# Optimization experiments

Hardware: AMD Instinct MI355X
Metric: run time of the kernel (lower is better)

The kernel has to match this reference:

```python
import jax, jax.numpy as jnp
import numpy as np
from jax import lax

B, N, HC = 16, 4096, 64
EPS = 1e-5


def _fps(xyz, npoint):
    # xyz: [B,N,3] -> indices [B,npoint]; deterministic start at index 0
    b, n, _ = xyz.shape
    def step(carry, _):
        dist, far = carry
        centroid = jnp.take_along_axis(xyz, far[:, None, None], axis=1)  # [B,1,3]
        d = jnp.sum((xyz - centroid) ** 2, -1)                           # [B,N]
        dist = jnp.minimum(dist, d)
        nxt = jnp.argmax(dist, -1).astype(jnp.int32)
        return (dist, nxt), far
    init = (jnp.full((b, n), 1e10, xyz.dtype), jnp.zeros((b,), jnp.int32))
    _, idx = lax.scan(step, init, None, length=npoint)
    return idx.T


def _index_points(pts, idx):
    # pts [B,N,C], idx [B,...] int -> [B,...,C]
    b = idx.shape[0]
    flat = jnp.take_along_axis(pts, idx.reshape(b, -1)[..., None], axis=1)
    return flat.reshape(idx.shape + (pts.shape[-1],))


def _ball_query(radius, nsample, xyz, new_xyz):
    # torch square_distance: ||a||^2 + ||b||^2 - 2 a.b
    n = xyz.shape[1]
    sqr = (jnp.sum(new_xyz ** 2, -1)[:, :, None] + jnp.sum(xyz ** 2, -1)[:, None, :]
           - 2.0 * jnp.einsum('bsd,bnd->bsn', new_xyz, xyz))          # [B,S,N]
    gi = jnp.where(sqr > radius ** 2, n, jnp.arange(n, dtype=jnp.int32))
    gi = jnp.sort(gi, axis=-1)[:, :, :nsample]
    first = gi[:, :, :1]
    return jnp.where(gi == n, first, gi)


def _mlp_maxpool(x, params):
    # x: [B,S,K,C]; 1x1 conv == per-point matmul; BN in training mode (batch stats)
    for (w, bb, g, be) in params:
        x = jnp.einsum('bskc,cd->bskd', x, w) + bb
        m = jnp.mean(x, axis=(0, 1, 2))
        v = jnp.var(x, axis=(0, 1, 2))
        x = g * (x - m) * lax.rsqrt(v + EPS) + be
        x = jax.nn.relu(x)
    return jnp.max(x, axis=2)  # [B,S,Cout]


def _sa(xyz, points, npoint, radius, nsample, params, group_all):
    # xyz [B,3,N], points [B,D,N] (channel-first, like torch)
    xyzt = jnp.transpose(xyz, (0, 2, 1))
    ptst = jnp.transpose(points, (0, 2, 1))
    if group_all:
        new_xyz = jnp.zeros((xyzt.shape[0], 1, 3), xyzt.dtype)
        new_pts = jnp.concatenate([xyzt[:, None], ptst[:, None]], -1)  # [B,1,N,3+D]
    else:
        fidx = _fps(xyzt, npoint)
        new_xyz = _index_points(xyzt, fidx)                            # [B,S,3]
        gi = _ball_query(radius, nsample, xyzt, new_xyz)               # [B,S,K]
        gxyz = _index_points(xyzt, gi) - new_xyz[:, :, None]           # [B,S,K,3]
        new_pts = jnp.concatenate([gxyz, _index_points(ptst, gi)], -1)
    feat = _mlp_maxpool(new_pts, params)                               # [B,S,Cout]
    return jnp.transpose(new_xyz, (0, 2, 1)), jnp.transpose(feat, (0, 2, 1))


def setup_inputs() -> dict:
    key = jax.random.key(0)
    ks = jax.random.split(key, 8)
    inp = {
        'l0_xyz': jax.random.normal(ks[0], (B, 3, N), jnp.float32),
        'l0_points': jax.random.normal(ks[1], (B, 3, N), jnp.float32),
    }
    dims = {'sa1': [(6, HC), (HC, HC * 2)],
            'sa2': [(HC * 2 + 3, HC * 2), (HC * 2, HC * 4)],
            'sa3': [(HC * 4 + 3, HC * 4), (HC * 4, HC * 8)]}
    i = 2
    for name, layers in dims.items():
        for j, (cin, cout) in enumerate(layers, 1):
            inp[f'{name}_w{j}'] = jax.random.normal(ks[i], (cin, cout), jnp.float32) * (1.0 / np.sqrt(cin))
            inp[f'{name}_b{j}'] = jnp.zeros((cout,), jnp.float32)
            inp[f'{name}_g{j}'] = jnp.ones((cout,), jnp.float32)
            inp[f'{name}_be{j}'] = jnp.zeros((cout,), jnp.float32)
            i += 1
    return inp


def reference(l0_xyz, l0_points,
              sa1_w1, sa1_b1, sa1_g1, sa1_be1, sa1_w2, sa1_b2, sa1_g2, sa1_be2,
              sa2_w1, sa2_b1, sa2_g1, sa2_be1, sa2_w2, sa2_b2, sa2_g2, sa2_be2,
              sa3_w1, sa3_b1, sa3_g1, sa3_be1, sa3_w2, sa3_b2, sa3_g2, sa3_be2):
    p1 = [(sa1_w1, sa1_b1, sa1_g1, sa1_be1), (sa1_w2, sa1_b2, sa1_g2, sa1_be2)]
    p2 = [(sa2_w1, sa2_b1, sa2_g1, sa2_be1), (sa2_w2, sa2_b2, sa2_g2, sa2_be2)]
    p3 = [(sa3_w1, sa3_b1, sa3_g1, sa3_be1), (sa3_w2, sa3_b2, sa3_g2, sa3_be2)]
    l1_xyz, l1_points = _sa(l0_xyz, l0_points, 256, 0.2, 32, p1, False)
    l2_xyz, l2_points = _sa(l1_xyz, l1_points, 128, 0.25, 64, p2, False)
    l3_xyz, l3_points = _sa(l2_xyz, l2_points, None, None, None, p3, True)
    x = l3_points.reshape(-1, HC * 8)
    return (l1_xyz, l1_points, l2_xyz, l2_points, l3_xyz, x)
```

## Files before the change

kernel.cpp:

```cpp
#include <hip/hip_runtime.h>
#include <cstddef>


#define EPSB 1e-5f
constexpr int SLOTS1 = 16;
constexpr int SLOTS2 = 64;
constexpr int BATCH = 16;

static __device__ __forceinline__ unsigned long long umax64(unsigned long long a,
                                                            unsigned long long b)
{
    return a > b ? a : b;
}

static __device__ __forceinline__ unsigned pack_bf16x2(float a, float b)
{
    unsigned ua = __float_as_uint(a), ub = __float_as_uint(b);
    ua += 0x7fffu + ((ua >> 16) & 1u);
    ub += 0x7fffu + ((ub >> 16) & 1u);
    return (ua >> 16) | (ub & 0xffff0000u);
}

static __device__ __forceinline__ unsigned short bf16_of(float a)
{
    unsigned u = __float_as_uint(a);
    u += 0x7fffu + ((u >> 16) & 1u);
    return (unsigned short)(u >> 16);
}

static __device__ __forceinline__ unsigned long long wave_umax64_dpp(unsigned long long x)
{
#define DPP_STEP(ctrl, rmask)                                                        \
    {                                                                                \
        int lo_ = __builtin_amdgcn_update_dpp(0, (int)(unsigned)x, ctrl, rmask, 0xf, false); \
        int hi_ = __builtin_amdgcn_update_dpp(0, (int)(unsigned)(x >> 32), ctrl, rmask, 0xf, false); \
        unsigned long long c_ = ((unsigned long long)(unsigned)hi_ << 32) | (unsigned)lo_; \
        x = umax64(x, c_);                                                           \
    }
    DPP_STEP(0x111, 0xf)
    DPP_STEP(0x112, 0xf)
    DPP_STEP(0x114, 0xf)
    DPP_STEP(0x118, 0xf)
    DPP_STEP(0x142, 0xa)
    DPP_STEP(0x143, 0xc)
#undef DPP_STEP
    unsigned lo = (unsigned)__builtin_amdgcn_readlane((int)(unsigned)x, 63);
    unsigned hi = (unsigned)__builtin_amdgcn_readlane((int)(unsigned)(x >> 32), 63);
    return ((unsigned long long)hi << 32) | lo;
}

template<int N, int NPOINT, int THREADS>
__device__ __forceinline__ void fps_body(char* smraw,
        const float* __restrict__ xyz, int bStride, int cStride, int nStride,
        int b, float* __restrict__ nxyz, float* __restrict__ lxyz)
{
    constexpr int PT = N / THREADS;
    constexpr int NW = THREADS / 64;
    const int t = threadIdx.x;
    float* sx = (float*)smraw;
    float* sy = sx + N;
    float* sz = sy + N;
    int* sel = (int*)(sz + N);
    unsigned long long* red = (unsigned long long*)(sel + NPOINT);
    const float* xb = xyz + (size_t)b * bStride;

    float px[PT], py[PT], pz[PT], dist[PT];
#pragma unroll
    for (int i = 0; i < PT; ++i) {
        int p = t + i * THREADS;
        px[i] = xb[(size_t)0 * cStride + (size_t)p * nStride];
        py[i] = xb[(size_t)1 * cStride + (size_t)p * nStride];
        pz[i] = xb[(size_t)2 * cStride + (size_t)p * nStride];
        sx[p] = px[i]; sy[p] = py[i]; sz[p] = pz[i];
        dist[i] = 1e10f;
    }
    if (t == 0) sel[0] = 0;
    if constexpr (NW > 1) __syncthreads();

    float cx = sx[0], cy = sy[0], cz = sz[0];
    for (int it = 1; it < NPOINT; ++it) {
        unsigned long long best = 0ull;
#pragma unroll
        for (int i = 0; i < PT; ++i) {
            float dx = px[i] - cx, dy = py[i] - cy, dz = pz[i] - cz;
            float d = __builtin_fmaf(dx, dx, __builtin_fmaf(dy, dy, dz * dz));
            float nd = fminf(dist[i], d);
            dist[i] = nd;
            unsigned long long k =
                ((unsigned long long)__float_as_uint(nd) << 32) |
                (unsigned int)(~(t + i * THREADS));
            best = umax64(best, k);
        }
        best = wave_umax64_dpp(best);
        int widx;
        if constexpr (NW > 1) {
            const int pb = it & 1;
            if ((t & 63) == 0) red[pb * NW + (t >> 6)] = best;
            __syncthreads();
            unsigned long long m = red[pb * NW + 0];
#pragma unroll
            for (int w = 1; w < NW; ++w) m = umax64(m, red[pb * NW + w]);
            widx = (int)(~(unsigned int)m);
        } else {
            widx = (int)(~(unsigned int)best);
        }
        if (t == 0) sel[it] = widx;
        cx = sx[widx]; cy = sy[widx]; cz = sz[widx];
    }
    if constexpr (NW > 1) __syncthreads();
    for (int s = t; s < NPOINT; s += THREADS) {
        int id = sel[s];
        float X = sx[id], Y = sy[id], Z = sz[id];
        nxyz[(size_t)(b * NPOINT + s) * 3 + 0] = X;
        nxyz[(size_t)(b * NPOINT + s) * 3 + 1] = Y;
        nxyz[(size_t)(b * NPOINT + s) * 3 + 2] = Z;
        lxyz[(size_t)b * 3 * NPOINT + 0 * NPOINT + s] = X;
        lxyz[(size_t)b * 3 * NPOINT + 1 * NPOINT + s] = Y;
        lxyz[(size_t)b * 3 * NPOINT + 2 * NPOINT + s] = Z;
    }
}

template<int COUTB>
__device__ __forceinline__ void proj_gemm_body(char* smraw, int blk,
        const float* __restrict__ xyzsrc, const float* __restrict__ featsrc,
        int N, int CF, const float* __restrict__ W, int coutFull,
        const float* __restrict__ bias, float* __restrict__ outp)
{
    constexpr int BK = 32, BKP = 36, TK = 4, TC = 4, THREADS = 512, ROWS = 64;
    constexpr int C2G = COUTB / TC;
    static_assert(C2G * (ROWS / TK) == THREADS, "thread shape");
    float (*al)[BKP] = (float (*)[BKP])smraw;
    float (*wl)[BKP] = (float (*)[BKP])(smraw + ROWS * BKP * 4);
    const int NCH = coutFull / COUTB;
    const int chunk = blk % NCH;
    const int rb = blk / NCH;
    const int m0 = rb * ROWS;
    const int c2_0 = chunk * COUTB;
    const int K = CF + 3;
    const int tid = threadIdx.x;
    const int c2g = tid % C2G, kt = tid / C2G;
    float acc[TK][TC];
#pragma unroll
    for (int i = 0; i < TK; ++i)
#pragma unroll
        for (int j = 0; j < TC; ++j) acc[i][j] = 0.f;
    const int npan = (K + BK - 1) / BK;
    for (int pan = 0; pan < npan; ++pan) {
        __syncthreads();
        const int cbase = pan * BK;
        for (int e = tid; e < ROWS * BK; e += THREADS) {
            int rl = e / BK, cl = e % BK;
            int c = cbase + cl;
            int m = m0 + rl;
            int bb = m / N, n = m % N;
            float v = 0.f;
            if (c < 3) v = xyzsrc[(size_t)(bb * N + n) * 3 + c];
            else if (c < K) v = featsrc[(size_t)(bb * N + n) * CF + (c - 3)];
            al[rl][cl] = v;
        }
        for (int e = tid; e < COUTB * BK; e += THREADS) {
            int c2 = e % COUTB, cl = e / COUTB;
            int c = cbase + cl;
            wl[c2][cl] = (c < K) ? W[(size_t)c * coutFull + c2_0 + c2] : 0.f;
        }
        __syncthreads();
#pragma unroll
        for (int cl = 0; cl < BK; cl += 4) {
            float4 av[TK], wv[TC];
#pragma unroll
            for (int i = 0; i < TK; ++i) av[i] = *(const float4*)&al[kt * TK + i][cl];
#pragma unroll
            for (int j = 0; j < TC; ++j) wv[j] = *(const float4*)&wl[c2g + j * C2G][cl];
#pragma unroll
            for (int i = 0; i < TK; ++i)
#pragma unroll
                for (int j = 0; j < TC; ++j)
                    acc[i][j] += av[i].x * wv[j].x + av[i].y * wv[j].y
                               + av[i].z * wv[j].z + av[i].w * wv[j].w;
        }
    }
#pragma unroll
    for (int j = 0; j < TC; ++j) {
        float bb_ = bias[c2_0 + c2g + j * C2G];
#pragma unroll
        for (int i = 0; i < TK; ++i) {
            int m = m0 + kt * TK + i;
            outp[(size_t)m * coutFull + c2_0 + c2g + j * C2G] = acc[i][j] + bb_;
        }
    }
}

__global__ __launch_bounds__(512)
void mega1_kernel(const float* __restrict__ l0_xyz, const float* __restrict__ l0_pts,
                  const float* __restrict__ w11, const float* __restrict__ b11,
                  float* __restrict__ p1,
                  float* __restrict__ nxyz1, float* __restrict__ o_l1xyz,
                  const float* __restrict__ w12, unsigned short* __restrict__ w12t,
                  const float* __restrict__ w22, unsigned short* __restrict__ w22t,
                  const float* __restrict__ w32, unsigned short* __restrict__ w32t,
                  float* __restrict__ stats)
{
    __shared__ __attribute__((aligned(16))) char arena[50304];
    int blk = blockIdx.x;
    const int tid = threadIdx.x;
    if (blk < 16) {
        fps_body<4096, 256, 512>(arena, l0_xyz, 3 * 4096, 4096, 1, blk, nxyz1, o_l1xyz);
        return;
    }
    blk -= 16;
    if (blk < 8192) {
        int idx = blk * 512 + tid;
        int d = idx & 63;
        int n = (idx >> 6) & 4095;
        int b = idx >> 18;
        const float* xb = l0_xyz + (size_t)b * 3 * 4096 + n;
        const float* pb = l0_pts + (size_t)b * 3 * 4096 + n;
        float a0 = xb[0], a1 = xb[4096], a2 = xb[2 * 4096];
        float a3 = pb[0], a4 = pb[4096], a5 = pb[2 * 4096];
        float acc = b11[d];
        acc += a0 * w11[d] + a1 * w11[64 + d] + a2 * w11[128 + d];
        acc += a3 * w11[192 + d] + a4 * w11[256 + d] + a5 * w11[320 + d];
        p1[idx] = acc;
        return;
    }
    blk -= 8192;
    if (blk < 16) {
        int i = blk * 512 + tid;
        if (i < 64 * 128) { int k = i / 128, n = i % 128; w12t[(size_t)n * 64 + k] = bf16_of(w12[i]); }
        return;
    }
    blk -= 16;
    if (blk < 64) {
        int i = blk * 512 + tid;
        if (i < 128 * 256) { int k = i / 256, n = i % 256; w22t[(size_t)n * 128 + k] = bf16_of(w22[i]); }
        return;
    }
    blk -= 64;
    if (blk < 256) {
        int i = blk * 512 + tid;
        if (i < 256 * 512) { int k = i / 512, n = i % 512; w32t[(size_t)n * 256 + k] = bf16_of(w32[i]); }
        return;
    }
    blk -= 256;
    {
        int i = blk * 512 + tid;
        if (i < 129024) stats[i] = 0.f;
    }
}

__global__ __launch_bounds__(512)
void mega2_kernel(const float* __restrict__ nxyz1, float* __restrict__ nxyz2,
                  float* __restrict__ o_l2xyz,
                  const float* __restrict__ feat1, const float* __restrict__ w21,
                  const float* __restrict__ b21, float* __restrict__ p2)
{
    __shared__ __attribute__((aligned(16))) char arena[27648];
    if (blockIdx.x < 16) {
        if (threadIdx.x < 64)
            fps_body<256, 128, 64>(arena, nxyz1, 768, 1, 3, blockIdx.x, nxyz2, o_l2xyz);
        return;
    }
    proj_gemm_body<128>(arena, blockIdx.x - 16, nxyz1, feat1, 256, 128, w21, 128, b21, p2);
}

__global__ __launch_bounds__(512)
void proj_gemm3_kernel(const float* __restrict__ xyzsrc, const float* __restrict__ featsrc,
                       int N, int CF, const float* __restrict__ W, int coutFull,
                       const float* __restrict__ bias, float* __restrict__ outp)
{
    __shared__ __attribute__((aligned(16))) char arena[27648];
    proj_gemm_body<128>(arena, blockIdx.x, xyzsrc, featsrc, N, CF, W, coutFull, bias, outp);
}

template<int NS, int D>
__global__ __launch_bounds__(64)
void ballstat_kernel(const float* __restrict__ xyz, int bStride, int cStride, int nStride, int N,
                     const float* __restrict__ nxyz, int S, float r2,
                     int* __restrict__ gi,
                     const float* __restrict__ W, float* __restrict__ q,
                     const float* __restrict__ p, float* __restrict__ slots)
{
    constexpr int DL = D / 64;
    __shared__ int sgo[NS];
    int bs = blockIdx.x;
    int b = bs / S;
    int l = threadIdx.x;
    float cx = nxyz[(size_t)bs * 3 + 0], cy = nxyz[(size_t)bs * 3 + 1], cz = nxyz[(size_t)bs * 3 + 2];
    float s2 = cx * cx + cy * cy + cz * cz;
    const float* xb = xyz + (size_t)b * bStride;
    int cnt = 0;
    int first = N - 1;
    int* go = gi + (size_t)bs * NS;
    for (int base = 0; base < N; base += 64) {
        int n = base + l;
        float x = xb[(size_t)0 * cStride + (size_t)n * nStride];
        float y = xb[(size_t)1 * cStride + (size_t)n * nStride];
        float z = xb[(size_t)2 * cStride + (size_t)n * nStride];
        float x2 = x * x + y * y + z * z;
        float dot = cx * x + cy * y + cz * z;
        float sqr = (s2 + x2) - 2.0f * dot;
        bool pass = (sqr <= r2);
        unsigned long long m = __ballot(pass);
        if (cnt == 0 && m) first = base + (__ffsll((unsigned long long)m) - 1);
        int pos = cnt + __popcll(m & ((1ull << l) - 1ull));
        if (pass && pos < NS) { go[pos] = n; sgo[pos] = n; }
        cnt += __popcll(m);
        if (cnt >= NS) break;
    }
    if (cnt < NS && l >= cnt && l < NS) { go[l] = first; sgo[l] = first; }

    float qv[DL];
#pragma unroll
    for (int j = 0; j < DL; ++j) {
        int d = j * 64 + l;
        qv[j] = cx * W[d] + cy * W[D + d] + cz * W[2 * D + d];
        q[(size_t)bs * D + d] = qv[j];
    }

    float s[DL], ss[DL];
#pragma unroll
    for (int j = 0; j < DL; ++j) { s[j] = 0.f; ss[j] = 0.f; }
    for (int k = 0; k < NS; ++k) {
        int idx = sgo[k];
        const float* pr = p + (size_t)(b * N + idx) * D;
#pragma unroll
        for (int j = 0; j < DL; ++j) {
            float v = pr[j * 64 + l] - qv[j];
            s[j] += v; ss[j] += v * v;
        }
    }
    int slot = bs & (SLOTS1 - 1);
#pragma unroll
    for (int j = 0; j < DL; ++j) {
        int d = j * 64 + l;
        atomicAdd(&slots[(size_t)(slot * 2 + 0) * D + d], s[j]);
        atomicAdd(&slots[(size_t)(slot * 2 + 1) * D + d], ss[j]);
    }
}

__global__ __launch_bounds__(256)
void stats_raw_kernel(const float* __restrict__ h, int M, int C, float* __restrict__ slots)
{
    int c = threadIdx.x;
    float sum = 0.f, sq = 0.f;
    for (int m = blockIdx.x; m < M; m += gridDim.x) {
        float v = h[(size_t)m * C + c];
        sum += v; sq += v * v;
    }
    int slot = blockIdx.x & (SLOTS1 - 1);
    atomicAdd(&slots[(size_t)(slot * 2 + 0) * C + c], sum);
    atomicAdd(&slots[(size_t)(slot * 2 + 1) * C + c], sq);
}

__global__ __launch_bounds__(256)
void bnfin_kernel(const float* __restrict__ st, int C, float cnt,
                  const float* __restrict__ g, const float* __restrict__ be,
                  float* __restrict__ sc, float* __restrict__ sh)
{
    int c = blockIdx.x * 256 + threadIdx.x;
    if (c >= C) return;
    float s0 = 0.f, s1 = 0.f;
    for (int sl = 0; sl < SLOTS1; ++sl) {
        s0 += st[(size_t)(sl * 2 + 0) * C + c];
        s1 += st[(size_t)(sl * 2 + 1) * C + c];
    }
    float mean = s0 / cnt;
    float var = s1 / cnt - mean * mean;
    float inv = 1.0f / sqrtf(var + EPSB);
    float s = g[c] * inv;
    sc[c] = s;
    sh[c] = be[c] - s * mean;
}

template<int KS, int CIN, int COUTB>
__global__ __launch_bounds__(512)
void mfma_gemm_kernel(const float* __restrict__ p, const float* __restrict__ q,
                      const int* __restrict__ gi, int S, int NCH, int N,
                      const float* __restrict__ bnsc, const float* __restrict__ bnsh,
                      const unsigned short* __restrict__ w2t, int coutFull,
                      const float* __restrict__ b2,
                      float* __restrict__ st2,
                      float* __restrict__ mx, float* __restrict__ mn)
{
    constexpr int MT = KS / 16;
    constexpr int NSL = 8 / MT;
    constexpr int SLW = COUTB / NSL;
    constexpr int TPW = SLW / 16;
    constexpr int KST = CIN / 32;
    constexpr int LDA = CIN + 8;
    typedef __attribute__((ext_vector_type(8))) short bf16x8;
    typedef __attribute__((ext_vector_type(4))) float f32x4;

    __shared__ __attribute__((aligned(16))) unsigned short hl[KS][LDA];
    __shared__ float red[4][8][SLW];

    const int chunk = blockIdx.x % NCH;
    const int bs = blockIdx.x / NCH;
    const int b = bs / S;
    const int tid = threadIdx.x;
    const int c2_0 = chunk * COUTB;
    const int w = tid >> 6, lane = tid & 63;
    const int mt = w % MT, ns = w / MT;
    const int lrow = lane & 15, quad = lane >> 4;

    constexpr int ITER = KS * CIN / (512 * 4);
    const int gbase = bs * KS;
#pragma unroll
    for (int it = 0; it < ITER; ++it) {
        int e = (it * 512 + tid) * 4;
        int k = e / CIN, c = e % CIN;
        int row = gi ? (b * N + gi[gbase + k]) : (b * KS + k);
        float4 v = *(const float4*)&p[(size_t)row * CIN + c];
        if (q) {
            float4 qq = *(const float4*)&q[(size_t)bs * CIN + c];
            v.x -= qq.x; v.y -= qq.y; v.z -= qq.z; v.w -= qq.w;
        }
        float4 sc = *(const float4*)&bnsc[c];
        float4 sh = *(const float4*)&bnsh[c];
        v.x = fmaxf(__builtin_fmaf(sc.x, v.x, sh.x), 0.f);
        v.y = fmaxf(__builtin_fmaf(sc.y, v.y, sh.y), 0.f);
        v.z = fmaxf(__builtin_fmaf(sc.z, v.z, sh.z), 0.f);
        v.w = fmaxf(__builtin_fmaf(sc.w, v.w, sh.w), 0.f);
        uint2 pk;
        pk.x = pack_bf16x2(v.x, v.y);
        pk.y = pack_bf16x2(v.z, v.w);
        *(uint2*)&hl[k][c] = pk;
    }
    __syncthreads();

    f32x4 acc[TPW];
#pragma unroll
    for (int t = 0; t < TPW; ++t) acc[t] = (f32x4){0.f, 0.f, 0.f, 0.f};

    const int nbase = c2_0 + ns * SLW + lrow;
#pragma unroll
    for (int ks = 0; ks < KST; ++ks) {
        bf16x8 a = *(const bf16x8*)&hl[mt * 16 + lrow][ks * 32 + quad * 8];
#pragma unroll
        for (int t = 0; t < TPW; ++t) {
            bf16x8 bfr = *(const bf16x8*)&w2t[(size_t)(nbase + t * 16) * CIN + ks * 32 + quad * 8];
            acc[t] = __builtin_amdgcn_mfma_f32_16x16x32_bf16(a, bfr, acc[t], 0, 0, 0);
        }
    }

#pragma unroll
    for (int t = 0; t < TPW; ++t) {
        float bias = b2[nbase + t * 16];
        float s = 0.f, sq = 0.f, amx = -3.4e38f, amn = 3.4e38f;
#pragma unroll
        for (int r = 0; r < 4; ++r) {
            float v = acc[t][r] + bias;
            s += v; sq += v * v;
            amx = fmaxf(amx, v); amn = fminf(amn, v);
        }
#pragma unroll
        for (int off = 16; off < 64; off <<= 1) {
            s += __shfl_xor(s, off);
            sq += __shfl_xor(sq, off);
            amx = fmaxf(amx, __shfl_xor(amx, off));
            amn = fminf(amn, __shfl_xor(amn, off));
        }
        if (quad == 0) {
            int lc = t * 16 + lrow;
            red[0][w][lc] = s; red[1][w][lc] = sq;
            red[2][w][lc] = amx; red[3][w][lc] = amn;
        }
    }
    __syncthreads();
    for (int c = tid; c < COUTB; c += 512) {
        int ns2 = c / SLW, lc = c % SLW;
        float s = 0.f, sq = 0.f, amx = -3.4e38f, amn = 3.4e38f;
#pragma unroll
        for (int m2 = 0; m2 < MT; ++m2) {
            int w2 = ns2 * MT + m2;
            s += red[0][w2][lc]; sq += red[1][w2][lc];
            amx = fmaxf(amx, red[2][w2][lc]);
            amn = fminf(amn, red[3][w2][lc]);
        }
        int slot = blockIdx.x & (SLOTS2 - 1);
        atomicAdd(&st2[(size_t)(slot * 2 + 0) * coutFull + c2_0 + c], s);
        atomicAdd(&st2[(size_t)(slot * 2 + 1) * coutFull + c2_0 + c], sq);
        mx[(size_t)bs * coutFull + c2_0 + c] = amx;
        mn[(size_t)bs * coutFull + c2_0 + c] = amn;
    }
}

__global__ __launch_bounds__(256)
void apply_kernel(const float* __restrict__ st2, int C, float m2count,
                  const float* __restrict__ g2, const float* __restrict__ be2,
                  const float* __restrict__ mx, const float* __restrict__ mn,
                  int S, float* __restrict__ feat, float* __restrict__ outT,
                  int total, float* __restrict__ zero48)
{
    __shared__ float sc[512], sh[512];
    for (int c = threadIdx.x; c < C; c += 256) {
        float s0 = 0.f, s1 = 0.f;
        for (int sl = 0; sl < SLOTS2; ++sl) {
            s0 += st2[(size_t)(sl * 2 + 0) * C + c];
            s1 += st2[(size_t)(sl * 2 + 1) * C + c];
        }
        float mean = s0 / m2count;
        float var = s1 / m2count - mean * mean;
        float inv = 1.0f / sqrtf(var + EPSB);
        float scl = g2[c] * inv;
        sc[c] = scl; sh[c] = be2[c] - scl * mean;
    }
    __syncthreads();
    if (zero48 && blockIdx.x == 0 && threadIdx.x < 48) zero48[threadIdx.x] = 0.f;
    for (int e = blockIdx.x * 256 + threadIdx.x; e < total; e += gridDim.x * 256) {
        int c = e % C;
        int s = (e / C) % S;
        int b = e / (C * S);
        float scl = sc[c];
        float v = (scl >= 0.f) ? mx[e] : mn[e];
        float y = fmaxf(scl * v + sh[c], 0.f);
        if (feat) feat[e] = y;
        outT[((size_t)b * C + c) * S + s] = y;
    }
}

extern "C" void kernel_launch(void* const* d_in, const int* in_sizes, int n_in,
                              void* d_out, int out_size, void* d_ws, size_t ws_size,
                              hipStream_t stream)
{
    (void)in_sizes; (void)n_in; (void)out_size; (void)ws_size;
    const float* l0_xyz = (const float*)d_in[0];
    const float* l0_pts = (const float*)d_in[1];
    const float* w11 = (const float*)d_in[2];  const float* b11 = (const float*)d_in[3];
    const float* g11 = (const float*)d_in[4];  const float* be11 = (const float*)d_in[5];
    const float* w12 = (const float*)d_in[6];  const float* b12 = (const float*)d_in[7];
    const float* g12 = (const float*)d_in[8];  const float* be12 = (const float*)d_in[9];
    const float* w21 = (const float*)d_in[10]; const float* b21 = (const float*)d_in[11];
    const float* g21 = (const float*)d_in[12]; const float* be21 = (const float*)d_in[13];
    const float* w22 = (const float*)d_in[14]; const float* b22 = (const float*)d_in[15];
    const float* g22 = (const float*)d_in[16]; const float* be22 = (const float*)d_in[17];
    const float* w31 = (const float*)d_in[18]; const float* b31 = (const float*)d_in[19];
    const float* g31 = (const float*)d_in[20]; const float* be31 = (const float*)d_in[21];
    const float* w32 = (const float*)d_in[22]; const float* b32 = (const float*)d_in[23];
    const float* g32 = (const float*)d_in[24]; const float* be32 = (const float*)d_in[25];

    float* out = (float*)d_out;
    float* o_l1xyz = out;
    float* o_l1pts = out + 12288;
    float* o_l2xyz = out + 536576;
    float* o_l2pts = out + 542720;
    float* o_l3xyz = out + 1067008;
    float* o_x     = out + 1067056;

    char* ws = (char*)d_ws;
    size_t off = 0;
    auto alloc = [&](size_t bytes) {
        void* r = ws + off;
        off += ((bytes + 255) & ~(size_t)255);
        return r;
    };
    float* nxyz1 = (float*)alloc(12288 * 4);
    float* nxyz2 = (float*)alloc(6144 * 4);
    int*   gi1   = (int*)alloc(131072 * 4);
    int*   gi2   = (int*)alloc(131072 * 4);
    float* p1    = (float*)alloc(4194304 * 4);
    float* q1    = (float*)alloc(262144 * 4);
    float* feat1 = (float*)alloc(524288 * 4);
    float* mx1   = (float*)alloc(524288 * 4);
    float* mn1   = (float*)alloc(524288 * 4);
    float* p2    = (float*)alloc(524288 * 4);
    float* q2    = (float*)alloc(262144 * 4);
    float* feat2 = (float*)alloc(524288 * 4);
    float* mx2   = (float*)alloc(524288 * 4);
    float* mn2   = (float*)alloc(524288 * 4);
    float* h31   = (float*)alloc(524288 * 4);
    float* mx3   = (float*)alloc(8192 * 4);
    float* mn3   = (float*)alloc(8192 * 4);
    float* stats = (float*)alloc(129024 * 4);
    float* st1a = stats;
    float* st2a = st1a + 2048;
    float* st1b = st2a + 16384;
    float* st2b = st1b + 4096;
    float* st3a = st2b + 32768;
    float* st3b = st3a + 8192;
    unsigned short* w12t = (unsigned short*)alloc(128 * 64 * 2);
    unsigned short* w22t = (unsigned short*)alloc(256 * 128 * 2);
    unsigned short* w32t = (unsigned short*)alloc(512 * 256 * 2);
    float* sc1 = (float*)alloc(64 * 4);   float* sh1 = (float*)alloc(64 * 4);
    float* sc2 = (float*)alloc(128 * 4);  float* sh2 = (float*)alloc(128 * 4);
    float* sc3 = (float*)alloc(256 * 4);  float* sh3 = (float*)alloc(256 * 4);

    mega1_kernel<<<8796, 512, 0, stream>>>(l0_xyz, l0_pts, w11, b11, p1,
                                           nxyz1, o_l1xyz,
                                           w12, w12t, w22, w22t, w32, w32t, stats);
    ballstat_kernel<32, 64><<<4096, 64, 0, stream>>>(l0_xyz, 3 * 4096, 4096, 1, 4096,
                                                     nxyz1, 256, 0.04f, gi1, w11, q1, p1, st1a);
    bnfin_kernel<<<1, 256, 0, stream>>>(st1a, 64, 131072.0f, g11, be11, sc1, sh1);
    mfma_gemm_kernel<32, 64, 128><<<4096, 512, 0, stream>>>(
        p1, q1, gi1, 256, 1, 4096, sc1, sh1, w12t, 128, b12, st2a, mx1, mn1);
    apply_kernel<<<128, 256, 0, stream>>>(st2a, 128, 131072.0f, g12, be12, mx1, mn1,
                                          256, feat1, o_l1pts, 524288, nullptr);

    mega2_kernel<<<80, 512, 0, stream>>>(nxyz1, nxyz2, o_l2xyz, feat1, w21, b21, p2);
    ballstat_kernel<64, 128><<<2048, 64, 0, stream>>>(nxyz1, 768, 1, 3, 256,
                                                      nxyz2, 128, 0.0625f, gi2, w21, q2, p2, st1b);
    bnfin_kernel<<<1, 256, 0, stream>>>(st1b, 128, 131072.0f, g21, be21, sc2, sh2);
    mfma_gemm_kernel<64, 128, 256><<<2048, 512, 0, stream>>>(
        p2, q2, gi2, 128, 1, 256, sc2, sh2, w22t, 256, b22, st2b, mx2, mn2);
    apply_kernel<<<128, 256, 0, stream>>>(st2b, 256, 131072.0f, g22, be22, mx2, mn2,
                                          128, feat2, o_l2pts, 524288, nullptr);

    proj_gemm3_kernel<<<64, 512, 0, stream>>>(nxyz2, feat2, 128, 256, w31, 256, b31, h31);
    stats_raw_kernel<<<128, 256, 0, stream>>>(h31, 2048, 256, st3a);
    bnfin_kernel<<<1, 256, 0, stream>>>(st3a, 256, 2048.0f, g31, be31, sc3, sh3);
    mfma_gemm_kernel<128, 256, 128><<<64, 512, 0, stream>>>(
        h31, nullptr, nullptr, 1, 4, 0, sc3, sh3, w32t, 512, b32, st3b, mx3, mn3);
    apply_kernel<<<32, 256, 0, stream>>>(st3b, 512, 2048.0f, g32, be32, mx3, mn3,
                                         1, nullptr, o_x, 8192, o_l3xyz);
}
```

Measured before the change: 567.2 us.

## Fuse BN finalize, apply and projection kernels; register-resident FPS with coordinate broadcast

FPS now tracks each candidate's coordinates in registers and passes the winning point's xyz through a small shared slot or readlane. This removes the shared-memory point arrays and the index-then-lookup step. The second-level FPS moves into the first ball-query launch, and BN finalization is folded into the GEMM and apply kernels, which removes the bnfin launches. The BN apply for each level is fused into the next level's projection GEMM together with its stats accumulation, dropping the feat buffers and the stats_raw kernel, which cuts launch count and intermediate traffic. In exchange, several blocks each recompute the BN scale/shift from the slot sums, and launch_bounds occupancy hints are added.

```diff
diff --git a/kernel.cpp b/kernel.cpp
--- a/kernel.cpp
+++ b/kernel.cpp
@@ -5,7 +5,6 @@
 #define EPSB 1e-5f
 constexpr int SLOTS1 = 16;
 constexpr int SLOTS2 = 64;
-constexpr int BATCH = 16;
 
 static __device__ __forceinline__ unsigned long long umax64(unsigned long long a,
                                                             unsigned long long b)
@@ -50,18 +49,15 @@
 }
 
 template<int N, int NPOINT, int THREADS>
-__device__ __forceinline__ void fps_body(char* smraw,
+__device__ __forceinline__ void fps_body(
+        unsigned long long* kslots, float4* cslots,
         const float* __restrict__ xyz, int bStride, int cStride, int nStride,
         int b, float* __restrict__ nxyz, float* __restrict__ lxyz)
 {
     constexpr int PT = N / THREADS;
     constexpr int NW = THREADS / 64;
+    constexpr int NSTASH = (NPOINT + THREADS - 1) / THREADS;
     const int t = threadIdx.x;
-    float* sx = (float*)smraw;
-    float* sy = sx + N;
-    float* sz = sy + N;
-    int* sel = (int*)(sz + N);
-    unsigned long long* red = (unsigned long long*)(sel + NPOINT);
     const float* xb = xyz + (size_t)b * bStride;
 
     float px[PT], py[PT], pz[PT], dist[PT];
@@ -71,126 +67,80 @@
         px[i] = xb[(size_t)0 * cStride + (size_t)p * nStride];
         py[i] = xb[(size_t)1 * cStride + (size_t)p * nStride];
         pz[i] = xb[(size_t)2 * cStride + (size_t)p * nStride];
-        sx[p] = px[i]; sy[p] = py[i]; sz[p] = pz[i];
         dist[i] = 1e10f;
     }
-    if (t == 0) sel[0] = 0;
-    if constexpr (NW > 1) __syncthreads();
-
-    float cx = sx[0], cy = sy[0], cz = sz[0];
+    float stx[NSTASH], sty[NSTASH], stz[NSTASH];
+#pragma unroll
+    for (int i = 0; i < NSTASH; ++i) { stx[i] = 0.f; sty[i] = 0.f; stz[i] = 0.f; }
+
+    float cx = xb[0], cy = xb[(size_t)cStride], cz = xb[(size_t)2 * cStride];
+    if (t == 0) { stx[0] = cx; sty[0] = cy; stz[0] = cz; }
+
     for (int it = 1; it < NPOINT; ++it) {
-        unsigned long long best = 0ull;
+        float bv = -1.0f; int bidx = 0; float bx = 0.f, by = 0.f, bz = 0.f;
 #pragma unroll
         for (int i = 0; i < PT; ++i) {
             float dx = px[i] - cx, dy = py[i] - cy, dz = pz[i] - cz;
             float d = __builtin_fmaf(dx, dx, __builtin_fmaf(dy, dy, dz * dz));
             float nd = fminf(dist[i], d);
             dist[i] = nd;
-            unsigned long long k =
-                ((unsigned long long)__float_as_uint(nd) << 32) |
-                (unsigned int)(~(t + i * THREADS));
-            best = umax64(best, k);
-        }
-        best = wave_umax64_dpp(best);
-        int widx;
+            bool g = nd > bv;
+            bv = g ? nd : bv;
+            bidx = g ? (t + i * THREADS) : bidx;
+            bx = g ? px[i] : bx; by = g ? py[i] : by; bz = g ? pz[i] : bz;
+        }
+        unsigned long long mykey =
+            ((unsigned long long)__float_as_uint(bv) << 32) | (unsigned)(~bidx);
+        unsigned long long wkey = wave_umax64_dpp(mykey);
+        float wx, wy, wz;
         if constexpr (NW > 1) {
             const int pb = it & 1;
-            if ((t & 63) == 0) red[pb * NW + (t >> 6)] = best;
+            if (mykey == wkey) {
+                kslots[pb * NW + (t >> 6)] = wkey;
+                cslots[pb * NW + (t >> 6)] = make_float4(bx, by, bz, 0.f);
+            }
             __syncthreads();
-            unsigned long long m = red[pb * NW + 0];
-#pragma unroll
-            for (int w = 1; w < NW; ++w) m = umax64(m, red[pb * NW + w]);
-            widx = (int)(~(unsigned int)m);
+            unsigned long long k[NW]; float4 cc[NW];
+#pragma unroll
+            for (int w = 0; w < NW; ++w) { k[w] = kslots[pb * NW + w]; cc[w] = cslots[pb * NW + w]; }
+#pragma unroll
+            for (int stp = 1; stp < NW; stp <<= 1)
+#pragma unroll
+                for (int w = 0; w < NW; w += 2 * stp)
+                    if (k[w + stp] > k[w]) { k[w] = k[w + stp]; cc[w] = cc[w + stp]; }
+            wkey = k[0]; wx = cc[0].x; wy = cc[0].y; wz = cc[0].z;
         } else {
-            widx = (int)(~(unsigned int)best);
-        }
-        if (t == 0) sel[it] = widx;
-        cx = sx[widx]; cy = sy[widx]; cz = sz[widx];
-    }
-    if constexpr (NW > 1) __syncthreads();
-    for (int s = t; s < NPOINT; s += THREADS) {
-        int id = sel[s];
-        float X = sx[id], Y = sy[id], Z = sz[id];
-        nxyz[(size_t)(b * NPOINT + s) * 3 + 0] = X;
-        nxyz[(size_t)(b * NPOINT + s) * 3 + 1] = Y;
-        nxyz[(size_t)(b * NPOINT + s) * 3 + 2] = Z;
-        lxyz[(size_t)b * 3 * NPOINT + 0 * NPOINT + s] = X;
-        lxyz[(size_t)b * 3 * NPOINT + 1 * NPOINT + s] = Y;
-        lxyz[(size_t)b * 3 * NPOINT + 2 * NPOINT + s] = Z;
-    }
-}
-
-template<int COUTB>
-__device__ __forceinline__ void proj_gemm_body(char* smraw, int blk,
-        const float* __restrict__ xyzsrc, const float* __restrict__ featsrc,
-        int N, int CF, const float* __restrict__ W, int coutFull,
-        const float* __restrict__ bias, float* __restrict__ outp)
-{
-    constexpr int BK = 32, BKP = 36, TK = 4, TC = 4, THREADS = 512, ROWS = 64;
-    constexpr int C2G = COUTB / TC;
-    static_assert(C2G * (ROWS / TK) == THREADS, "thread shape");
-    float (*al)[BKP] = (float (*)[BKP])smraw;
-    float (*wl)[BKP] = (float (*)[BKP])(smraw + ROWS * BKP * 4);
-    const int NCH = coutFull / COUTB;
-    const int chunk = blk % NCH;
-    const int rb = blk / NCH;
-    const int m0 = rb * ROWS;
-    const int c2_0 = chunk * COUTB;
-    const int K = CF + 3;
-    const int tid = threadIdx.x;
-    const int c2g = tid % C2G, kt = tid / C2G;
-    float acc[TK][TC];
-#pragma unroll
-    for (int i = 0; i < TK; ++i)
-#pragma unroll
-        for (int j = 0; j < TC; ++j) acc[i][j] = 0.f;
-    const int npan = (K + BK - 1) / BK;
-    for (int pan = 0; pan < npan; ++pan) {
-        __syncthreads();
-        const int cbase = pan * BK;
-        for (int e = tid; e < ROWS * BK; e += THREADS) {
-            int rl = e / BK, cl = e % BK;
-            int c = cbase + cl;
-            int m = m0 + rl;
-            int bb = m / N, n = m % N;
-            float v = 0.f;
-            if (c < 3) v = xyzsrc[(size_t)(bb * N + n) * 3 + c];
-            else if (c < K) v = featsrc[(size_t)(bb * N + n) * CF + (c - 3)];
-            al[rl][cl] = v;
-        }
-        for (int e = tid; e < COUTB * BK; e += THREADS) {
-            int c2 = e % COUTB, cl = e / COUTB;
-            int c = cbase + cl;
-            wl[c2][cl] = (c < K) ? W[(size_t)c * coutFull + c2_0 + c2] : 0.f;
-        }
-        __syncthreads();
-#pragma unroll
-        for (int cl = 0; cl < BK; cl += 4) {
-            float4 av[TK], wv[TC];
-#pragma unroll
-            for (int i = 0; i < TK; ++i) av[i] = *(const float4*)&al[kt * TK + i][cl];
-#pragma unroll
-            for (int j = 0; j < TC; ++j) wv[j] = *(const float4*)&wl[c2g + j * C2G][cl];
-#pragma unroll
-            for (int i = 0; i < TK; ++i)
-#pragma unroll
-                for (int j = 0; j < TC; ++j)
-                    acc[i][j] += av[i].x * wv[j].x + av[i].y * wv[j].y
-                               + av[i].z * wv[j].z + av[i].w * wv[j].w;
-        }
-    }
-#pragma unroll
-    for (int j = 0; j < TC; ++j) {
-        float bb_ = bias[c2_0 + c2g + j * C2G];
-#pragma unroll
-        for (int i = 0; i < TK; ++i) {
-            int m = m0 + kt * TK + i;
-            outp[(size_t)m * coutFull + c2_0 + c2g + j * C2G] = acc[i][j] + bb_;
-        }
-    }
-}
-
-__global__ __launch_bounds__(512)
+            unsigned long long ball = __ballot(mykey == wkey);
+            int wl = __ffsll(ball) - 1;
+            wx = __int_as_float(__builtin_amdgcn_readlane(__float_as_int(bx), wl));
+            wy = __int_as_float(__builtin_amdgcn_readlane(__float_as_int(by), wl));
+            wz = __int_as_float(__builtin_amdgcn_readlane(__float_as_int(bz), wl));
+        }
+        if constexpr (NSTASH == 1) {
+            if (t == it) { stx[0] = wx; sty[0] = wy; stz[0] = wz; }
+        } else {
+            if ((it & (THREADS - 1)) == t) {
+                if (it >= THREADS) { stx[1] = wx; sty[1] = wy; stz[1] = wz; }
+                else               { stx[0] = wx; sty[0] = wy; stz[0] = wz; }
+            }
+        }
+        cx = wx; cy = wy; cz = wz;
+    }
+#pragma unroll
+    for (int s2 = 0; s2 < NSTASH; ++s2) {
+        int s = t + s2 * THREADS;
+        if (s < NPOINT) {
+            nxyz[(size_t)(b * NPOINT + s) * 3 + 0] = stx[s2];
+            nxyz[(size_t)(b * NPOINT + s) * 3 + 1] = sty[s2];
+            nxyz[(size_t)(b * NPOINT + s) * 3 + 2] = stz[s2];
+            lxyz[(size_t)b * 3 * NPOINT + 0 * NPOINT + s] = stx[s2];
+            lxyz[(size_t)b * 3 * NPOINT + 1 * NPOINT + s] = sty[s2];
+            lxyz[(size_t)b * 3 * NPOINT + 2 * NPOINT + s] = stz[s2];
+        }
+    }
+}
+
+__global__ __launch_bounds__(512, 2)
 void mega1_kernel(const float* __restrict__ l0_xyz, const float* __restrict__ l0_pts,
                   const float* __restrict__ w11, const float* __restrict__ b11,
                   float* __restrict__ p1,
@@ -200,11 +150,12 @@
                   const float* __restrict__ w32, unsigned short* __restrict__ w32t,
                   float* __restrict__ stats)
 {
-    __shared__ __attribute__((aligned(16))) char arena[50304];
+    __shared__ unsigned long long kxs[16];
+    __shared__ float4 cxs[16];
     int blk = blockIdx.x;
     const int tid = threadIdx.x;
     if (blk < 16) {
-        fps_body<4096, 256, 512>(arena, l0_xyz, 3 * 4096, 4096, 1, blk, nxyz1, o_l1xyz);
+        fps_body<4096, 256, 512>(kxs, cxs, l0_xyz, 3 * 4096, 4096, 1, blk, nxyz1, o_l1xyz);
         return;
     }
     blk -= 16;
@@ -248,41 +199,25 @@
     }
 }
 
-__global__ __launch_bounds__(512)
-void mega2_kernel(const float* __restrict__ nxyz1, float* __restrict__ nxyz2,
-                  float* __restrict__ o_l2xyz,
-                  const float* __restrict__ feat1, const float* __restrict__ w21,
-                  const float* __restrict__ b21, float* __restrict__ p2)
-{
-    __shared__ __attribute__((aligned(16))) char arena[27648];
-    if (blockIdx.x < 16) {
-        if (threadIdx.x < 64)
-            fps_body<256, 128, 64>(arena, nxyz1, 768, 1, 3, blockIdx.x, nxyz2, o_l2xyz);
-        return;
-    }
-    proj_gemm_body<128>(arena, blockIdx.x - 16, nxyz1, feat1, 256, 128, w21, 128, b21, p2);
-}
-
-__global__ __launch_bounds__(512)
-void proj_gemm3_kernel(const float* __restrict__ xyzsrc, const float* __restrict__ featsrc,
-                       int N, int CF, const float* __restrict__ W, int coutFull,
-                       const float* __restrict__ bias, float* __restrict__ outp)
-{
-    __shared__ __attribute__((aligned(16))) char arena[27648];
-    proj_gemm_body<128>(arena, blockIdx.x, xyzsrc, featsrc, N, CF, W, coutFull, bias, outp);
-}
-
-template<int NS, int D>
-__global__ __launch_bounds__(64)
+template<int NS, int D, bool WITHFPS>
+__global__ __launch_bounds__(64, 4)
 void ballstat_kernel(const float* __restrict__ xyz, int bStride, int cStride, int nStride, int N,
                      const float* __restrict__ nxyz, int S, float r2,
                      int* __restrict__ gi,
                      const float* __restrict__ W, float* __restrict__ q,
-                     const float* __restrict__ p, float* __restrict__ slots)
-{
+                     const float* __restrict__ p, float* __restrict__ slots,
+                     const float* __restrict__ fxyz, float* __restrict__ fnxyz,
+                     float* __restrict__ flxyz)
+{
+    if constexpr (WITHFPS) {
+        if (blockIdx.x < 16) {
+            fps_body<256, 128, 64>(nullptr, nullptr, fxyz, 768, 1, 3, blockIdx.x, fnxyz, flxyz);
+            return;
+        }
+    }
     constexpr int DL = D / 64;
     __shared__ int sgo[NS];
-    int bs = blockIdx.x;
+    int bs = blockIdx.x - (WITHFPS ? 16 : 0);
     int b = bs / S;
     int l = threadIdx.x;
     float cx = nxyz[(size_t)bs * 3 + 0], cy = nxyz[(size_t)bs * 3 + 1], cz = nxyz[(size_t)bs * 3 + 2];
@@ -316,7 +251,6 @@
         qv[j] = cx * W[d] + cy * W[D + d] + cz * W[2 * D + d];
         q[(size_t)bs * D + d] = qv[j];
     }
-
     float s[DL], ss[DL];
 #pragma unroll
     for (int j = 0; j < DL; ++j) { s[j] = 0.f; ss[j] = 0.f; }
@@ -338,45 +272,12 @@
     }
 }
 
-__global__ __launch_bounds__(256)
-void stats_raw_kernel(const float* __restrict__ h, int M, int C, float* __restrict__ slots)
-{
-    int c = threadIdx.x;
-    float sum = 0.f, sq = 0.f;
-    for (int m = blockIdx.x; m < M; m += gridDim.x) {
-        float v = h[(size_t)m * C + c];
-        sum += v; sq += v * v;
-    }
-    int slot = blockIdx.x & (SLOTS1 - 1);
-    atomicAdd(&slots[(size_t)(slot * 2 + 0) * C + c], sum);
-    atomicAdd(&slots[(size_t)(slot * 2 + 1) * C + c], sq);
-}
-
-__global__ __launch_bounds__(256)
-void bnfin_kernel(const float* __restrict__ st, int C, float cnt,
-                  const float* __restrict__ g, const float* __restrict__ be,
-                  float* __restrict__ sc, float* __restrict__ sh)
-{
-    int c = blockIdx.x * 256 + threadIdx.x;
-    if (c >= C) return;
-    float s0 = 0.f, s1 = 0.f;
-    for (int sl = 0; sl < SLOTS1; ++sl) {
-        s0 += st[(size_t)(sl * 2 + 0) * C + c];
-        s1 += st[(size_t)(sl * 2 + 1) * C + c];
-    }
-    float mean = s0 / cnt;
-    float var = s1 / cnt - mean * mean;
-    float inv = 1.0f / sqrtf(var + EPSB);
-    float s = g[c] * inv;
-    sc[c] = s;
-    sh[c] = be[c] - s * mean;
-}
-
 template<int KS, int CIN, int COUTB>
-__global__ __launch_bounds__(512)
+__global__ __launch_bounds__(512, 2)
 void mfma_gemm_kernel(const float* __restrict__ p, const float* __restrict__ q,
                       const int* __restrict__ gi, int S, int NCH, int N,
-                      const float* __restrict__ bnsc, const float* __restrict__ bnsh,
+                      const float* __restrict__ st1, float m1cnt,
+                      const float* __restrict__ g1, const float* __restrict__ be1,
                       const unsigned short* __restrict__ w2t, int coutFull,
                       const float* __restrict__ b2,
                       float* __restrict__ st2,
@@ -393,6 +294,8 @@
 
     __shared__ __attribute__((aligned(16))) unsigned short hl[KS][LDA];
     __shared__ float red[4][8][SLW];
+    __shared__ __attribute__((aligned(16))) float ss_scale[CIN];
+    __shared__ __attribute__((aligned(16))) float ss_shift[CIN];
 
     const int chunk = blockIdx.x % NCH;
     const int bs = blockIdx.x / NCH;
@@ -403,6 +306,21 @@
     const int mt = w % MT, ns = w / MT;
     const int lrow = lane & 15, quad = lane >> 4;
 
+    for (int c = tid; c < CIN; c += 512) {
+        float s0 = 0.f, s1 = 0.f;
+        for (int sl = 0; sl < SLOTS1; ++sl) {
+            s0 += st1[(size_t)(sl * 2 + 0) * CIN + c];
+            s1 += st1[(size_t)(sl * 2 + 1) * CIN + c];
+        }
+        float mean = s0 / m1cnt;
+        float var = s1 / m1cnt - mean * mean;
+        float inv = 1.0f / sqrtf(var + EPSB);
+        float scl = g1[c] * inv;
+        ss_scale[c] = scl;
+        ss_shift[c] = be1[c] - scl * mean;
+    }
+    __syncthreads();
+
     constexpr int ITER = KS * CIN / (512 * 4);
     const int gbase = bs * KS;
 #pragma unroll
@@ -415,8 +333,8 @@
             float4 qq = *(const float4*)&q[(size_t)bs * CIN + c];
             v.x -= qq.x; v.y -= qq.y; v.z -= qq.z; v.w -= qq.w;
         }
-        float4 sc = *(const float4*)&bnsc[c];
-        float4 sh = *(const float4*)&bnsh[c];
+        float4 sc = *(const float4*)&ss_scale[c];
+        float4 sh = *(const float4*)&ss_shift[c];
         v.x = fmaxf(__builtin_fmaf(sc.x, v.x, sh.x), 0.f);
         v.y = fmaxf(__builtin_fmaf(sc.y, v.y, sh.y), 0.f);
         v.z = fmaxf(__builtin_fmaf(sc.z, v.z, sh.z), 0.f);
@@ -485,38 +403,197 @@
     }
 }
 
-__global__ __launch_bounds__(256)
-void apply_kernel(const float* __restrict__ st2, int C, float m2count,
-                  const float* __restrict__ g2, const float* __restrict__ be2,
-                  const float* __restrict__ mx, const float* __restrict__ mn,
-                  int S, float* __restrict__ feat, float* __restrict__ outT,
-                  int total, float* __restrict__ zero48)
-{
-    __shared__ float sc[512], sh[512];
-    for (int c = threadIdx.x; c < C; c += 256) {
+__device__ __forceinline__ void apply_body(char* smraw, int blk, int nblk,
+        const float* __restrict__ st2, int C, float cnt,
+        const float* __restrict__ g2, const float* __restrict__ be2,
+        const float* __restrict__ mx, const float* __restrict__ mn,
+        int S, float* __restrict__ outT, int total, float* __restrict__ zero48)
+{
+    float* sc = (float*)smraw;
+    float* sh = sc + 512;
+    for (int c = threadIdx.x; c < C; c += 512) {
         float s0 = 0.f, s1 = 0.f;
         for (int sl = 0; sl < SLOTS2; ++sl) {
             s0 += st2[(size_t)(sl * 2 + 0) * C + c];
             s1 += st2[(size_t)(sl * 2 + 1) * C + c];
         }
-        float mean = s0 / m2count;
-        float var = s1 / m2count - mean * mean;
+        float mean = s0 / cnt;
+        float var = s1 / cnt - mean * mean;
         float inv = 1.0f / sqrtf(var + EPSB);
         float scl = g2[c] * inv;
         sc[c] = scl; sh[c] = be2[c] - scl * mean;
     }
     __syncthreads();
-    if (zero48 && blockIdx.x == 0 && threadIdx.x < 48) zero48[threadIdx.x] = 0.f;
-    for (int e = blockIdx.x * 256 + threadIdx.x; e < total; e += gridDim.x * 256) {
-        int c = e % C;
-        int s = (e / C) % S;
-        int b = e / (C * S);
+    if (zero48 && blk == 0 && threadIdx.x < 48) zero48[threadIdx.x] = 0.f;
+    for (int e = blk * 512 + threadIdx.x; e < total; e += nblk * 512) {
+        int s = e % S;
+        int rem = e / S;
+        int c = rem % C;
+        int b = rem / C;
         float scl = sc[c];
-        float v = (scl >= 0.f) ? mx[e] : mn[e];
-        float y = fmaxf(scl * v + sh[c], 0.f);
-        if (feat) feat[e] = y;
-        outT[((size_t)b * C + c) * S + s] = y;
-    }
+        size_t mi = (size_t)(b * S + s) * C + c;
+        float v = (scl >= 0.f) ? mx[mi] : mn[mi];
+        outT[e] = fmaxf(scl * v + sh[c], 0.f);
+    }
+}
+
+template<int COUTB, bool DOSTATS>
+__device__ __forceinline__ void proj_body(char* smraw, int blk,
+        const float* __restrict__ xyzsrc,
+        const float* __restrict__ mxF, const float* __restrict__ mnF,
+        const float* __restrict__ stF, const float* __restrict__ gF,
+        const float* __restrict__ beF, float cntF,
+        int N, int CF, const float* __restrict__ W, int coutFull,
+        const float* __restrict__ bias, float* __restrict__ outp,
+        float* __restrict__ st3)
+{
+    constexpr int BK = 32, BKP = 36, TK = 4, TC = 4, THREADS = 512, ROWS = 64;
+    constexpr int C2G = COUTB / TC;
+    float (*al)[BKP] = (float (*)[BKP])smraw;
+    float (*wl)[BKP] = (float (*)[BKP])(smraw + ROWS * BKP * 4);
+    float* scF = (float*)(smraw + (ROWS + COUTB) * BKP * 4);
+    float* shF = scF + CF;
+    float* red2 = shF + CF;
+    const int NCH = coutFull / COUTB;
+    const int chunk = blk % NCH;
+    const int rb = blk / NCH;
+    const int m0 = rb * ROWS;
+    const int c2_0 = chunk * COUTB;
+    const int K = CF + 3;
+    const int tid = threadIdx.x;
+    const int c2g = tid % C2G, kt = tid / C2G;
+
+    for (int c = tid; c < CF; c += THREADS) {
+        float s0 = 0.f, s1 = 0.f;
+        for (int sl = 0; sl < SLOTS2; ++sl) {
+            s0 += stF[(size_t)(sl * 2 + 0) * CF + c];
+            s1 += stF[(size_t)(sl * 2 + 1) * CF + c];
+        }
+        float mean = s0 / cntF;
+        float var = s1 / cntF - mean * mean;
+        float inv = 1.0f / sqrtf(var + EPSB);
+        float scl = gF[c] * inv;
+        scF[c] = scl; shF[c] = beF[c] - scl * mean;
+    }
+
+    float acc[TK][TC];
+#pragma unroll
+    for (int i = 0; i < TK; ++i)
+#pragma unroll
+        for (int j = 0; j < TC; ++j) acc[i][j] = 0.f;
+    const int npan = (K + BK - 1) / BK;
+    for (int pan = 0; pan < npan; ++pan) {
+        __syncthreads();
+        const int cbase = pan * BK;
+        for (int e = tid; e < ROWS * BK; e += THREADS) {
+            int rl = e / BK, cl = e % BK;
+            int c = cbase + cl;
+            int m = m0 + rl;
+            float v = 0.f;
+            if (c < 3) v = xyzsrc[(size_t)m * 3 + c];
+            else if (c < K) {
+                int cf = c - 3;
+                float scl = scF[cf];
+                size_t mi = (size_t)m * CF + cf;
+                float pick = (scl >= 0.f) ? mxF[mi] : mnF[mi];
+                v = fmaxf(scl * pick + shF[cf], 0.f);
+            }
+            al[rl][cl] = v;
+        }
+        for (int e = tid; e < COUTB * BK; e += THREADS) {
+            int c2 = e % COUTB, cl = e / COUTB;
+            int c = cbase + cl;
+            wl[c2][cl] = (c < K) ? W[(size_t)c * coutFull + c2_0 + c2] : 0.f;
+        }
+        __syncthreads();
+#pragma unroll
+        for (int cl = 0; cl < BK; cl += 4) {
+            float4 av[TK], wv[TC];
+#pragma unroll
+            for (int i = 0; i < TK; ++i) av[i] = *(const float4*)&al[kt * TK + i][cl];
+#pragma unroll
+            for (int j = 0; j < TC; ++j) wv[j] = *(const float4*)&wl[c2g + j * C2G][cl];
+#pragma unroll
+            for (int i = 0; i < TK; ++i)
+#pragma unroll
+                for (int j = 0; j < TC; ++j)
+                    acc[i][j] += av[i].x * wv[j].x + av[i].y * wv[j].y
+                               + av[i].z * wv[j].z + av[i].w * wv[j].w;
+        }
+    }
+    float ps[TC], pq[TC];
+#pragma unroll
+    for (int j = 0; j < TC; ++j) {
+        float bb_ = bias[c2_0 + c2g + j * C2G];
+        float s = 0.f, sq = 0.f;
+#pragma unroll
+        for (int i = 0; i < TK; ++i) {
+            int m = m0 + kt * TK + i;
+            float v = acc[i][j] + bb_;
+            outp[(size_t)m * coutFull + c2_0 + c2g + j * C2G] = v;
+            s += v; sq += v * v;
+        }
+        ps[j] = s; pq[j] = sq;
+    }
+    if constexpr (DOSTATS) {
+        const int w = tid >> 6, lane = tid & 63;
+#pragma unroll
+        for (int j = 0; j < TC; ++j) {
+            ps[j] += __shfl_xor(ps[j], 32);
+            pq[j] += __shfl_xor(pq[j], 32);
+            if (lane < 32) {
+                int c2 = c2g + j * C2G;
+                red2[(w * COUTB + c2) * 2 + 0] = ps[j];
+                red2[(w * COUTB + c2) * 2 + 1] = pq[j];
+            }
+        }
+        __syncthreads();
+        for (int c = tid; c < COUTB; c += THREADS) {
+            float s = 0.f, sq = 0.f;
+#pragma unroll
+            for (int w2 = 0; w2 < 8; ++w2) {
+                s += red2[(w2 * COUTB + c) * 2 + 0];
+                sq += red2[(w2 * COUTB + c) * 2 + 1];
+            }
+            int slot = blk & (SLOTS1 - 1);
+            atomicAdd(&st3[(size_t)(slot * 2 + 0) * coutFull + c2_0 + c], s);
+            atomicAdd(&st3[(size_t)(slot * 2 + 1) * coutFull + c2_0 + c], sq);
+        }
+    }
+}
+
+template<bool DOSTATS>
+__global__ __launch_bounds__(512, 2)
+void applyproj_kernel(
+        const float* __restrict__ xyzsrc,
+        const float* __restrict__ mxF, const float* __restrict__ mnF,
+        const float* __restrict__ stF, const float* __restrict__ gF,
+        const float* __restrict__ beF, float cntF,
+        int Nrows, int CF, const float* __restrict__ W, int coutFull,
+        const float* __restrict__ bias, float* __restrict__ outp,
+        float* __restrict__ st3, int projBlocks,
+        const float* __restrict__ st2, int C, float m2cnt,
+        const float* __restrict__ g2, const float* __restrict__ be2,
+        const float* __restrict__ mxA, const float* __restrict__ mnA,
+        int S, float* __restrict__ outT, int total)
+{
+    __shared__ __attribute__((aligned(16))) char arena[38144];
+    if ((int)blockIdx.x < projBlocks)
+        proj_body<128, DOSTATS>(arena, blockIdx.x, xyzsrc, mxF, mnF, stF, gF, beF, cntF,
+                                Nrows, CF, W, coutFull, bias, outp, st3);
+    else
+        apply_body(arena, blockIdx.x - projBlocks, gridDim.x - projBlocks,
+                   st2, C, m2cnt, g2, be2, mxA, mnA, S, outT, total, nullptr);
+}
+
+__global__ __launch_bounds__(512, 2)
+void apply3_kernel(const float* __restrict__ st2, int C, float cnt,
+                   const float* __restrict__ g2, const float* __restrict__ be2,
+                   const float* __restrict__ mx, const float* __restrict__ mn,
+                   int S, float* __restrict__ outT, int total, float* __restrict__ zero48)
+{
+    __shared__ __attribute__((aligned(16))) char arena[4160];
+    apply_body(arena, blockIdx.x, gridDim.x, st2, C, cnt, g2, be2, mx, mn, S, outT, total, zero48);
 }
 
 extern "C" void kernel_launch(void* const* d_in, const int* in_sizes, int n_in,
@@ -560,12 +637,10 @@
     int*   gi2   = (int*)alloc(131072 * 4);
     float* p1    = (float*)alloc(4194304 * 4);
     float* q1    = (float*)alloc(262144 * 4);
-    float* feat1 = (float*)alloc(524288 * 4);
     float* mx1   = (float*)alloc(524288 * 4);
     float* mn1   = (float*)alloc(524288 * 4);
     float* p2    = (float*)alloc(524288 * 4);
     float* q2    = (float*)alloc(262144 * 4);
-    float* feat2 = (float*)alloc(524288 * 4);
     float* mx2   = (float*)alloc(524288 * 4);
     float* mn2   = (float*)alloc(524288 * 4);
     float* h31   = (float*)alloc(524288 * 4);
@@ -581,35 +656,33 @@
     unsigned short* w12t = (unsigned short*)alloc(128 * 64 * 2);
     unsigned short* w22t = (unsigned short*)alloc(256 * 128 * 2);
     unsigned short* w32t = (unsigned short*)alloc(512 * 256 * 2);
-    float* sc1 = (float*)alloc(64 * 4);   float* sh1 = (float*)alloc(64 * 4);
-    float* sc2 = (float*)alloc(128 * 4);  float* sh2 = (float*)alloc(128 * 4);
-    float* sc3 = (float*)alloc(256 * 4);  float* sh3 = (float*)alloc(256 * 4);
 
     mega1_kernel<<<8796, 512, 0, stream>>>(l0_xyz, l0_pts, w11, b11, p1,
                                            nxyz1, o_l1xyz,
                                            w12, w12t, w22, w22t, w32, w32t, stats);
-    ballstat_kernel<32, 64><<<4096, 64, 0, stream>>>(l0_xyz, 3 * 4096, 4096, 1, 4096,
-                                                     nxyz1, 256, 0.04f, gi1, w11, q1, p1, st1a);
-    bnfin_kernel<<<1, 256, 0, stream>>>(st1a, 64, 131072.0f, g11, be11, sc1, sh1);
+    ballstat_kernel<32, 64, true><<<4112, 64, 0, stream>>>(
+        l0_xyz, 3 * 4096, 4096, 1, 4096, nxyz1, 256, 0.04f, gi1, w11, q1, p1, st1a,
+        nxyz1, nxyz2, o_l2xyz);
     mfma_gemm_kernel<32, 64, 128><<<4096, 512, 0, stream>>>(
-        p1, q1, gi1, 256, 1, 4096, sc1, sh1, w12t, 128, b12, st2a, mx1, mn1);
-    apply_kernel<<<128, 256, 0, stream>>>(st2a, 128, 131072.0f, g12, be12, mx1, mn1,
-                                          256, feat1, o_l1pts, 524288, nullptr);
-
-    mega2_kernel<<<80, 512, 0, stream>>>(nxyz1, nxyz2, o_l2xyz, feat1, w21, b21, p2);
-    ballstat_kernel<64, 128><<<2048, 64, 0, stream>>>(nxyz1, 768, 1, 3, 256,
-                                                      nxyz2, 128, 0.0625f, gi2, w21, q2, p2, st1b);
-    bnfin_kernel<<<1, 256, 0, stream>>>(st1b, 128, 131072.0f, g21, be21, sc2, sh2);
+        p1, q1, gi1, 256, 1, 4096, st1a, 131072.0f, g11, be11, w12t, 128, b12,
+        st2a, mx1, mn1);
+    applyproj_kernel<false><<<128, 512, 0, stream>>>(
+        nxyz1, mx1, mn1, st2a, g12, be12, 131072.0f, 256, 128, w21, 128, b21, p2,
+        nullptr, 64,
+        st2a, 128, 131072.0f, g12, be12, mx1, mn1, 256, o_l1pts, 524288);
+    ballstat_kernel<64, 128, false><<<2048, 64, 0, stream>>>(
+        nxyz1, 768, 1, 3, 256, nxyz2, 128, 0.0625f, gi2, w21, q2, p2, st1b,
+        nullptr, nullptr, nullptr);
     mfma_gemm_kernel<64, 128, 256><<<2048, 512, 0, stream>>>(
-        p2, q2, gi2, 128, 1, 256, sc2, sh2, w22t, 256, b22, st2b, mx2, mn2);
-    apply_kernel<<<128, 256, 0, stream>>>(st2b, 256, 131072.0f, g22, be22, mx2, mn2,
-                                          128, feat2, o_l2pts, 524288, nullptr);
-
-    proj_gemm3_kernel<<<64, 512, 0, stream>>>(nxyz2, feat2, 128, 256, w31, 256, b31, h31);
-    stats_raw_kernel<<<128, 256, 0, stream>>>(h31, 2048, 256, st3a);
-    bnfin_kernel<<<1, 256, 0, stream>>>(st3a, 256, 2048.0f, g31, be31, sc3, sh3);
+        p2, q2, gi2, 128, 1, 256, st1b, 131072.0f, g21, be21, w22t, 256, b22,
+        st2b, mx2, mn2);
+    applyproj_kernel<true><<<128, 512, 0, stream>>>(
+        nxyz2, mx2, mn2, st2b, g22, be22, 131072.0f, 128, 256, w31, 256, b31, h31,
+        st3a, 64,
+        st2b, 256, 131072.0f, g22, be22, mx2, mn2, 128, o_l2pts, 524288);
     mfma_gemm_kernel<128, 256, 128><<<64, 512, 0, stream>>>(
-        h31, nullptr, nullptr, 1, 4, 0, sc3, sh3, w32t, 512, b32, st3b, mx3, mn3);
-    apply_kernel<<<32, 256, 0, stream>>>(st3b, 512, 2048.0f, g32, be32, mx3, mn3,
-                                         1, nullptr, o_x, 8192, o_l3xyz);
-}
+        h31, nullptr, nullptr, 1, 4, 0, st3a, 2048.0f, g31, be31, w32t, 512, b32,
+        st3b, mx3, mn3);
+    apply3_kernel<<<16, 512, 0, stream>>>(st3b, 512, 2048.0f, g32, be32, mx3, mn3,
+                                          1, o_x, 8192, o_l3xyz);
+}
```

New measurement: 660.1 us. 16.4% more time.
